# Performance work log

Measured on AMD Instinct MI355X. Metric: run time of the kernel, lower is better.

Reference implementation:

```python
import jax, jax.numpy as jnp
import numpy as np
import math

HEAD_SIZE = 64
WINDOW = 512  # sliding_window_size


def setup_inputs() -> dict:
    key = jax.random.key(0)
    k1, k2, k3, k4 = jax.random.split(key, 4)
    B, T, C = 4, 4096, 1024
    x = jax.random.normal(k1, (B, T, C), dtype=jnp.float32)
    # torch nn.Linear(C, head_size, bias=False) computes x @ W.T with W [hs, C];
    # we store the transposed [C, hs] layout so projection is x @ w.
    s = 1.0 / math.sqrt(C)
    w_key = jax.random.uniform(k2, (C, HEAD_SIZE), jnp.float32, -s, s)
    w_query = jax.random.uniform(k3, (C, HEAD_SIZE), jnp.float32, -s, s)
    w_value = jax.random.uniform(k4, (C, HEAD_SIZE), jnp.float32, -s, s)
    return {"x": x, "w_key": w_key, "w_query": w_query, "w_value": w_value}


def reference(x, w_key, w_query, w_value):
    # Non-cache path (use_cache=False): keys/values are the fresh projections,
    # q_start = k_start = 0, win_size = sliding_window_size.
    B, T, C = x.shape
    q = x @ w_query          # [B, T, hs]
    k = x @ w_key            # [B, T, hs]
    v = x @ w_value          # [B, T, hs]

    # attn_scores = q @ k^T  -> [B, T, T]
    scores = jnp.einsum('btd,bsd->bts', q, k)

    # Sliding-window causal mask: invalid where diff < 0 or diff >= window,
    # with diff = q_pos - k_pos.
    pos = jnp.arange(T)
    diff = pos[:, None] - pos[None, :]          # [T, T]
    mask_bool = (diff < 0) | (diff >= WINDOW)

    scale = math.sqrt(HEAD_SIZE)
    scores = jnp.where(mask_bool[None, :, :], -jnp.inf, scores)
    attn = jax.nn.softmax(scores / scale, axis=-1)  # dropout p=0.0 -> identity

    out = jnp.einsum('bts,bsd->btd', attn, v)   # [B, T, hs]
    return out
```

## Files before the change

kernel.cpp:

```cpp
#include <hip/hip_runtime.h>
#include <hip/hip_bf16.h>
#include <math.h>

#define BB 4
#define TT 4096
#define CC 1024
#define HS 64
#define WIN 512
#define NROW (BB*TT)

typedef float f32x4 __attribute__((ext_vector_type(4)));
typedef short bf16x8 __attribute__((ext_vector_type(8)));

#define MFMA16(a, b, c) __builtin_amdgcn_mfma_f32_16x16x32_bf16((a), (b), (c), 0, 0, 0)

#define GLOAD_LDS(gp, lp) __builtin_amdgcn_global_load_lds( \
    (const __attribute__((address_space(1))) void*)(gp), \
    (__attribute__((address_space(3))) void*)(lp), 16, 0, 0)

__device__ inline unsigned short f2b(float f) {
  union { __hip_bfloat16 h; unsigned short u; } v;
  v.h = __float2bfloat16(f);
  return v.u;
}

__global__ __launch_bounds__(256) void pack_w_kernel(
    const float* __restrict__ wq, const float* __restrict__ wk,
    const float* __restrict__ wv, unsigned short* __restrict__ wp)
{
  int t = blockIdx.x * 256 + threadIdx.x;
  int kg = t / 48;
  int nq = t % 48;
  int n0 = nq * 4;
  int m  = n0 >> 6;
  int c  = n0 & 63;
  const float* w = (m == 0) ? wq : (m == 1) ? wk : wv;
  float4 v = *(const float4*)&w[(size_t)kg * HS + c];
  int kt = kg >> 5;
  int hi = (kg >> 3) & 3;
  int j  = kg & 7;
  float vals[4] = {v.x, v.y, v.z, v.w};
  #pragma unroll
  for (int i = 0; i < 4; ++i) {
    int n  = n0 + i;
    int nb = n >> 4;
    int rl = n & 15;
    int lane = hi * 16 + rl;
    wp[((size_t)(kt * 12 + nb) * 64 + lane) * 8 + j] = f2b(vals[i]);
  }
}

__global__ __launch_bounds__(512) void proj_mfma_kernel(
    const float* __restrict__ x, const unsigned short* __restrict__ wp,
    unsigned short* __restrict__ q_ws, unsigned short* __restrict__ k_ws,
    unsigned short* __restrict__ vt_ws)
{
  __shared__ unsigned char lds[131072];
  unsigned char* const xb0 = lds;
  unsigned char* const xb1 = lds + 16384;
  unsigned char* const wb0 = lds + 32768;
  unsigned char* const wb1 = lds + 81920;

  const int tid = threadIdx.x;
  const int l   = tid & 63;
  const int wid = tid >> 6;
  const int cq  = wid & 3;
  const int rh  = wid >> 2;
  const int rl  = l & 15;
  const int hi  = l >> 4;
  const int r0  = blockIdx.x * 64;

  f32x4 acc[2][3];
  #pragma unroll
  for (int g = 0; g < 2; ++g)
    #pragma unroll
    for (int j = 0; j < 3; ++j) acc[g][j] = (f32x4){0.f, 0.f, 0.f, 0.f};

  f32x4 xr[2][2];

#define SXL(KS) { \
    _Pragma("unroll") \
    for (int it = 0; it < 2; ++it) { \
      int u = it * 512 + tid; \
      const float* gp = x + (size_t)(r0 + (u >> 4)) * CC + (KS) * 128 + (u & 15) * 8; \
      xr[it][0] = *(const f32x4*)gp; \
      xr[it][1] = *(const f32x4*)(gp + 4); \
    } }

#define XPACK(XB) { \
    _Pragma("unroll") \
    for (int it = 0; it < 2; ++it) { \
      int u = it * 512 + tid; \
      int row = u >> 4, seg = u & 15; \
      uint4 pk; \
      pk.x = (unsigned)f2b(xr[it][0][0]) | ((unsigned)f2b(xr[it][0][1]) << 16); \
      pk.y = (unsigned)f2b(xr[it][0][2]) | ((unsigned)f2b(xr[it][0][3]) << 16); \
      pk.z = (unsigned)f2b(xr[it][1][0]) | ((unsigned)f2b(xr[it][1][1]) << 16); \
      pk.w = (unsigned)f2b(xr[it][1][2]) | ((unsigned)f2b(xr[it][1][3]) << 16); \
      *(uint4*)((XB) + row * 256 + (((seg ^ (row & 7))) << 4)) = pk; \
    } }

#define SW(KS, WB) { \
    const unsigned short* wsrc = wp + (size_t)(KS) * 24576; \
    _Pragma("unroll") \
    for (int i = 0; i < 6; ++i) { \
      int s = i * 512 + tid; \
      GLOAD_LDS(wsrc + s * 8, (WB) + s * 16); \
    } }

#define COMP(XB, WB) { \
    _Pragma("unroll") \
    for (int kt = 0; kt < 4; ++kt) { \
      bf16x8 afr[2]; \
      _Pragma("unroll") \
      for (int g = 0; g < 2; ++g) { \
        int row = rh * 32 + g * 16 + rl; \
        int seg = kt * 4 + hi; \
        afr[g] = *(const bf16x8*)((XB) + row * 256 + ((seg ^ (row & 7)) << 4)); \
      } \
      _Pragma("unroll") \
      for (int j = 0; j < 3; ++j) { \
        bf16x8 wf = *(const bf16x8*)((WB) + ((kt * 12 + cq * 3 + j) * 64 + l) * 16); \
        acc[0][j] = MFMA16(afr[0], wf, acc[0][j]); \
        acc[1][j] = MFMA16(afr[1], wf, acc[1][j]); \
      } \
    } }

  SXL(0)
  SW(0, wb0)
  XPACK(xb0)
  __syncthreads();

  #pragma unroll
  for (int ks = 0; ks < 8; ++ks) {
    unsigned char* const xc = (ks & 1) ? xb1 : xb0;
    unsigned char* const wc = (ks & 1) ? wb1 : wb0;
    unsigned char* const xn = (ks & 1) ? xb0 : xb1;
    unsigned char* const wn = (ks & 1) ? wb0 : wb1;
    if (ks < 7) { SXL(ks + 1) SW(ks + 1, wn) }
    COMP(xc, wc)
    if (ks < 7) { XPACK(xn) }
    __syncthreads();
  }
#undef SXL
#undef XPACK
#undef SW
#undef COMP

  #pragma unroll
  for (int g = 0; g < 2; ++g) {
    int rb = r0 + rh * 32 + g * 16;
    #pragma unroll
    for (int j = 0; j < 3; ++j) {
      int nb = cq * 3 + j;
      if (nb < 8) {
        unsigned short* dst = (nb < 4) ? q_ws : k_ws;
        int c = (nb & 3) * 16 + rl;
        #pragma unroll
        for (int r = 0; r < 4; ++r) {
          int row = rb + hi * 4 + r;
          dst[(size_t)row * HS + c] = f2b(acc[g][j][r]);
        }
      } else {
        int ch   = rb >> 6;
        int key0 = (rb & 63) + hi * 4;
        int d = (nb - 8) * 16 + rl;
        unsigned u0 = (unsigned)f2b(acc[g][j][0]) | ((unsigned)f2b(acc[g][j][1]) << 16);
        unsigned u1 = (unsigned)f2b(acc[g][j][2]) | ((unsigned)f2b(acc[g][j][3]) << 16);
        uint2 uu; uu.x = u0; uu.y = u1;
        *(uint2*)(vt_ws + (size_t)ch * 4096 + d * 64 + key0) = uu;
      }
    }
  }
}

__global__ __launch_bounds__(256) void attn_mfma_kernel(
    const unsigned short* __restrict__ q_ws, const unsigned short* __restrict__ k_ws,
    const unsigned short* __restrict__ vt_ws, float* __restrict__ out)
{
  __shared__ uint4 smem4[1600];
  unsigned char* smem = (unsigned char*)smem4;

  const int tid = threadIdx.x;
  const int l   = tid & 63;
  const int wid = tid >> 6;
  const int rl  = l & 15;
  const int hi  = l >> 4;
  const int b   = blockIdx.x >> 6;
  const int qt  = blockIdx.x & 63;
  const int t0  = qt * 64;
  const int t0w = t0 + wid * 16;

  const unsigned short* qrow = q_ws + (size_t)(b * TT + t0w + rl) * HS;
  bf16x8 qb0 = *(const bf16x8*)(qrow + hi * 8);
  bf16x8 qb1 = *(const bf16x8*)(qrow + 32 + hi * 8);

  f32x4 oacc[4];
  #pragma unroll
  for (int i = 0; i < 4; ++i) oacc[i] = (f32x4){0.f, 0.f, 0.f, 0.f};
  float m_run = -INFINITY, l_run = 0.f;

  int s_lo = t0 - WIN; if (s_lo < 0) s_lo = 0;
  unsigned char* pbase = smem + 16384 + wid * 2304 + rl * 144;

  for (int sc = s_lo; sc < t0 + 64; sc += 64) {
    __syncthreads();
    {
      const unsigned short* kg = k_ws + (size_t)(b * TT + sc) * HS;
      const unsigned short* vg = vt_ws + (size_t)((b * TT + sc) >> 6) * 4096;
      #pragma unroll
      for (int i = 0; i < 2; ++i) {
        int idx = tid + i * 256;
        int row = idx >> 3;
        int c16 = idx & 7;
        uint4 kv = *(const uint4*)(kg + row * 64 + c16 * 8);
        uint4 vv = *(const uint4*)(vg + row * 64 + c16 * 8);
        *(uint4*)(smem + row * 128 + ((c16 ^ (row & 7)) * 16)) = kv;
        *(uint4*)(smem + 8192 + row * 128 + ((c16 ^ (row & 7)) * 16)) = vv;
      }
    }
    __syncthreads();

    f32x4 sacc[4];
    #pragma unroll
    for (int i = 0; i < 4; ++i) sacc[i] = (f32x4){0.f, 0.f, 0.f, 0.f};
    #pragma unroll
    for (int kb = 0; kb < 4; ++kb) {
      int row = kb * 16 + rl;
      unsigned char* kr = smem + row * 128;
      bf16x8 k0 = *(const bf16x8*)(kr + (((hi) ^ (row & 7)) * 16));
      bf16x8 k1 = *(const bf16x8*)(kr + (((4 + hi) ^ (row & 7)) * 16));
      sacc[kb] = MFMA16(k0, qb0, sacc[kb]);
      sacc[kb] = MFMA16(k1, qb1, sacc[kb]);
    }

    const int tg = t0w + rl;
    float p[16];
    float tm = -INFINITY;
    bool full = (sc + 63 <= t0w) && (sc >= t0w - 496);
    #pragma unroll
    for (int kb = 0; kb < 4; ++kb)
      #pragma unroll
      for (int r = 0; r < 4; ++r) {
        float v = sacc[kb][r] * 0.125f;
        if (!full) {
          int key = sc + kb * 16 + hi * 4 + r;
          int diff = tg - key;
          v = (diff >= 0 && diff < WIN) ? v : -INFINITY;
        }
        p[kb * 4 + r] = v;
        tm = fmaxf(tm, v);
      }
    tm = fmaxf(tm, __shfl_xor(tm, 16));
    tm = fmaxf(tm, __shfl_xor(tm, 32));
    float m_new = fmaxf(m_run, tm);
    float fac  = (m_new == -INFINITY) ? 1.f : __expf(m_run - m_new);
    float msub = (m_new == -INFINITY) ? 0.f : m_new;
    float lsum = 0.f;
    #pragma unroll
    for (int i = 0; i < 16; ++i) { p[i] = __expf(p[i] - msub); lsum += p[i]; }
    lsum += __shfl_xor(lsum, 16);
    lsum += __shfl_xor(lsum, 32);
    l_run = l_run * fac + lsum;
    m_run = m_new;

    #pragma unroll
    for (int kb = 0; kb < 4; ++kb) {
      unsigned u0 = (unsigned)f2b(p[kb * 4 + 0]) | ((unsigned)f2b(p[kb * 4 + 1]) << 16);
      unsigned u1 = (unsigned)f2b(p[kb * 4 + 2]) | ((unsigned)f2b(p[kb * 4 + 3]) << 16);
      uint2 uu; uu.x = u0; uu.y = u1;
      *(uint2*)(pbase + kb * 32 + hi * 8) = uu;
    }

    #pragma unroll
    for (int r = 0; r < 4; ++r) {
      float fr = __shfl(fac, (l & 48) | (hi * 4 + r));
      oacc[0][r] *= fr; oacc[1][r] *= fr; oacc[2][r] *= fr; oacc[3][r] *= fr;
    }

    bf16x8 pa0 = *(const bf16x8*)(pbase + hi * 16);
    bf16x8 pa1 = *(const bf16x8*)(pbase + 64 + hi * 16);
    #pragma unroll
    for (int f = 0; f < 4; ++f) {
      int d = f * 16 + rl;
      unsigned char* vr = smem + 8192 + d * 128;
      bf16x8 v0 = *(const bf16x8*)(vr + (((hi) ^ (d & 7)) * 16));
      bf16x8 v1 = *(const bf16x8*)(vr + (((4 + hi) ^ (d & 7)) * 16));
      oacc[f] = MFMA16(pa0, v0, oacc[f]);
      oacc[f] = MFMA16(pa1, v1, oacc[f]);
    }
  }

  float inv = 1.f / l_run;
  #pragma unroll
  for (int r = 0; r < 4; ++r) {
    float ir = __shfl(inv, (l & 48) | (hi * 4 + r));
    int row = b * TT + t0w + hi * 4 + r;
    #pragma unroll
    for (int f = 0; f < 4; ++f)
      out[(size_t)row * HS + f * 16 + rl] = oacc[f][r] * ir;
  }
}

extern "C" void kernel_launch(void* const* d_in, const int* in_sizes, int n_in,
                              void* d_out, int out_size, void* d_ws, size_t ws_size,
                              hipStream_t stream) {
  const float* x  = (const float*)d_in[0];
  const float* wk = (const float*)d_in[1];
  const float* wq = (const float*)d_in[2];
  const float* wv = (const float*)d_in[3];
  float* out = (float*)d_out;

  unsigned short* wp    = (unsigned short*)d_ws;
  unsigned short* q_ws  = wp + 196608;
  unsigned short* k_ws  = q_ws + (size_t)NROW * HS;
  unsigned short* vt_ws = k_ws + (size_t)NROW * HS;

  pack_w_kernel<<<192, 256, 0, stream>>>(wq, wk, wv, wp);
  proj_mfma_kernel<<<NROW / 64, 512, 0, stream>>>(x, wp, q_ws, k_ws, vt_ws);
  attn_mfma_kernel<<<BB * (TT / 64), 256, 0, stream>>>(q_ws, k_ws, vt_ws, out);
}
```

Before: 44.56 us.

## Split attention KV range across two blocks and merge with a reduce kernel

Each query tile's sliding-window key range is now split into two halves, each handled by its own block, which doubles the attention grid. Each half writes an unnormalized partial output plus its running max and sum to workspace. A new reduce kernel then combines the two halves with log-sum-exp rescaling. The aim is more parallelism and shorter per-block serial loops, at the cost of an extra kernel launch and extra global traffic for the partial results.

```diff
diff --git a/kernel.cpp b/kernel.cpp
--- a/kernel.cpp
+++ b/kernel.cpp
@@ -176,7 +176,8 @@
 
 __global__ __launch_bounds__(256) void attn_mfma_kernel(
     const unsigned short* __restrict__ q_ws, const unsigned short* __restrict__ k_ws,
-    const unsigned short* __restrict__ vt_ws, float* __restrict__ out)
+    const unsigned short* __restrict__ vt_ws,
+    float* __restrict__ op_ws, float* __restrict__ ml_ws)
 {
   __shared__ uint4 smem4[1600];
   unsigned char* smem = (unsigned char*)smem4;
@@ -186,8 +187,10 @@
   const int wid = tid >> 6;
   const int rl  = l & 15;
   const int hi  = l >> 4;
-  const int b   = blockIdx.x >> 6;
-  const int qt  = blockIdx.x & 63;
+  const int split = blockIdx.x & 1;
+  const int bq  = blockIdx.x >> 1;
+  const int b   = bq >> 6;
+  const int qt  = bq & 63;
   const int t0  = qt * 64;
   const int t0w = t0 + wid * 16;
 
@@ -201,9 +204,14 @@
   float m_run = -INFINITY, l_run = 0.f;
 
   int s_lo = t0 - WIN; if (s_lo < 0) s_lo = 0;
+  const int nch = (t0 + 64 - s_lo) >> 6;
+  const int h   = nch >> 1;
+  const int c_lo = split ? (s_lo + h * 64) : s_lo;
+  const int c_hi = split ? (t0 + 64) : (s_lo + h * 64);
+
   unsigned char* pbase = smem + 16384 + wid * 2304 + rl * 144;
 
-  for (int sc = s_lo; sc < t0 + 64; sc += 64) {
+  for (int sc = c_lo; sc < c_hi; sc += 64) {
     __syncthreads();
     {
       const unsigned short* kg = k_ws + (size_t)(b * TT + sc) * HS;
@@ -291,15 +299,38 @@
     }
   }
 
-  float inv = 1.f / l_run;
   #pragma unroll
   for (int r = 0; r < 4; ++r) {
-    float ir = __shfl(inv, (l & 48) | (hi * 4 + r));
-    int row = b * TT + t0w + hi * 4 + r;
+    size_t gq = (size_t)(b * TT + t0w + hi * 4 + r);
     #pragma unroll
     for (int f = 0; f < 4; ++f)
-      out[(size_t)row * HS + f * 16 + rl] = oacc[f][r] * ir;
-  }
+      op_ws[(gq * 2 + split) * HS + f * 16 + rl] = oacc[f][r];
+  }
+  if (hi == 0) {
+    size_t gq = (size_t)(b * TT + t0w + rl);
+    ml_ws[gq * 4 + split * 2 + 0] = m_run;
+    ml_ws[gq * 4 + split * 2 + 1] = l_run;
+  }
+}
+
+__global__ __launch_bounds__(256) void reduce_kernel(
+    const float* __restrict__ op_ws, const float* __restrict__ ml_ws,
+    float* __restrict__ out)
+{
+  int gid = blockIdx.x * 256 + threadIdx.x;
+  int r  = gid >> 4;
+  int c4 = (gid & 15) * 4;
+  float4 mlv = *(const float4*)&ml_ws[(size_t)r * 4];
+  float M  = fmaxf(mlv.x, mlv.z);
+  float a0 = __expf(mlv.x - M);
+  float a1 = __expf(mlv.z - M);
+  float inv = 1.f / (a0 * mlv.y + a1 * mlv.w);
+  f32x4 o0 = *(const f32x4*)&op_ws[((size_t)r * 2 + 0) * HS + c4];
+  f32x4 o1 = *(const f32x4*)&op_ws[((size_t)r * 2 + 1) * HS + c4];
+  f32x4 o;
+  #pragma unroll
+  for (int i = 0; i < 4; ++i) o[i] = (o0[i] * a0 + o1[i] * a1) * inv;
+  *(f32x4*)&out[(size_t)r * HS + c4] = o;
 }
 
 extern "C" void kernel_launch(void* const* d_in, const int* in_sizes, int n_in,
@@ -315,8 +346,11 @@
   unsigned short* q_ws  = wp + 196608;
   unsigned short* k_ws  = q_ws + (size_t)NROW * HS;
   unsigned short* vt_ws = k_ws + (size_t)NROW * HS;
+  float* op_ws = (float*)(vt_ws + (size_t)NROW * HS);
+  float* ml_ws = op_ws + (size_t)NROW * 2 * HS;
 
   pack_w_kernel<<<192, 256, 0, stream>>>(wq, wk, wv, wp);
   proj_mfma_kernel<<<NROW / 64, 512, 0, stream>>>(x, wp, q_ws, k_ws, vt_ws);
-  attn_mfma_kernel<<<BB * (TT / 64), 256, 0, stream>>>(q_ws, k_ws, vt_ws, out);
-}
+  attn_mfma_kernel<<<BB * (TT / 64) * 2, 256, 0, stream>>>(q_ws, k_ws, vt_ws, op_ws, ml_ws);
+  reduce_kernel<<<NROW * HS / 4 / 256, 256, 0, stream>>>(op_ws, ml_ws, out);
+}
```

Measured after the change: 41.76 us. -6.3%, faster.
